# Kernel tuning notes

Hardware: AMD Instinct MI355X
Metric: run time of the kernel (lower is better)

The kernel has to match this reference:

```python
import jax, jax.numpy as jnp
import numpy as np
import math

EMBED = 1024
HEADS = 16
HEAD_DIM = EMBED // HEADS
WINDOW = 128
B, S = 2, 2048


def setup_inputs() -> dict:
    key = jax.random.key(0)
    k1, k2, k3, k4 = jax.random.split(key, 4)
    values = jax.random.normal(k1, (B, S, EMBED), dtype=jnp.float32)
    keys = jax.random.normal(k2, (B, S, EMBED), dtype=jnp.float32)
    queries = jax.random.normal(k3, (B, S, EMBED), dtype=jnp.float32)
    # sliding-window band mask: 1 where |i-j| <= WINDOW//2, else 0
    idx = jnp.arange(S)
    band = (jnp.abs(idx[:, None] - idx[None, :]) <= WINDOW // 2).astype(jnp.int32)
    mask = band[None, None, :, :]  # [1,1,S,S], broadcasts over batch and heads
    w_out = jax.random.normal(k4, (EMBED, EMBED), dtype=jnp.float32) * (1.0 / math.sqrt(EMBED))
    b_out = jnp.zeros((EMBED,), dtype=jnp.float32)
    return {"values": values, "keys": keys, "queries": queries, "mask": mask,
            "w_out": w_out, "b_out": b_out}


def reference(values, keys, queries, mask, w_out, b_out):
    N, q_len = queries.shape[0], queries.shape[1]
    v = values.reshape(N, -1, HEADS, HEAD_DIM)
    k = keys.reshape(N, -1, HEADS, HEAD_DIM)
    q = queries.reshape(N, -1, HEADS, HEAD_DIM)
    # dense N x N energy, as in the original (no windowed blocking)
    energy = jnp.einsum('nqhd,nkhd->nhqk', q, k)
    energy = jnp.where(mask == 0, jnp.float32(-1e20), energy)
    attn = jax.nn.softmax(energy / math.sqrt(EMBED), axis=3)
    out = jnp.einsum('nhql,nlhd->nqhd', attn, v).reshape(N, q_len, HEADS * HEAD_DIM)
    return out @ w_out.T + b_out
```

## Files before the change

### kernel.cpp

```cpp
#include <hip/hip_runtime.h>

typedef __bf16 bf16x8 __attribute__((ext_vector_type(8)));
typedef float floatx4 __attribute__((ext_vector_type(4)));
typedef unsigned short ushortx8 __attribute__((ext_vector_type(8)));
typedef unsigned short ushortx4 __attribute__((ext_vector_type(4)));
typedef unsigned short ushort_t;

#define SB 2048
#define EB 1024
#define HB 16
#define DB 64
#define QT 64
#define KBAND 192
#define KROW 72
#define VROW 200

__device__ __forceinline__ ushort_t f2bf(float f) {
    union { float f; unsigned int u; } v; v.f = f;
    unsigned int r = v.u + 0x7fffu + ((v.u >> 16) & 1u);
    return (ushort_t)(r >> 16);
}

union BF8 { ushortx8 u; bf16x8 b; };

__global__ __launch_bounds__(256) void cvtw_kernel(const float* __restrict__ w,
                                                   ushort_t* __restrict__ wb) {
    int i = blockIdx.x * 256 + threadIdx.x;
    const float4 v = ((const float4*)w)[i];
    ushortx4 o;
    o.x = f2bf(v.x); o.y = f2bf(v.y); o.z = f2bf(v.z); o.w = f2bf(v.w);
    ((ushortx4*)wb)[i] = o;
}

__global__ __launch_bounds__(256) void attn_kernel(const float* __restrict__ Vg,
                                                   const float* __restrict__ Kg,
                                                   const float* __restrict__ Qg,
                                                   ushort_t* __restrict__ Xg) {
    __shared__ ushort_t Klds[KBAND * KROW];
    __shared__ ushort_t Vt[DB * VROW];

    const int tid  = threadIdx.x;
    const int wave = tid >> 6;
    const int lane = tid & 63;
    const int l15  = lane & 15;
    const int l4   = lane >> 4;

    const int qt = blockIdx.x & 31;
    const int h  = (blockIdx.x >> 5) & 15;
    const int b  = blockIdx.x >> 9;

    const int q0     = qt * QT;
    const int kstart = q0 - 64;

    const float* Kbase = Kg + ((size_t)b * SB) * EB + h * DB;
    const float* Vbase = Vg + ((size_t)b * SB) * EB + h * DB;

    #pragma unroll
    for (int it = 0; it < (KBAND * DB / 4) / 256; ++it) {
        int idx = it * 256 + tid;
        int j   = idx >> 4;
        int d4  = (idx & 15) * 4;
        int kk  = kstart + j;
        float4 kv = make_float4(0.f, 0.f, 0.f, 0.f);
        float4 vv = make_float4(0.f, 0.f, 0.f, 0.f);
        if (kk >= 0 && kk < SB) {
            kv = *(const float4*)(Kbase + (size_t)kk * EB + d4);
            vv = *(const float4*)(Vbase + (size_t)kk * EB + d4);
        }
        ushortx4 ku;
        ku.x = f2bf(kv.x); ku.y = f2bf(kv.y); ku.z = f2bf(kv.z); ku.w = f2bf(kv.w);
        *(ushortx4*)(Klds + j * KROW + d4) = ku;
        Vt[(d4 + 0) * VROW + j] = f2bf(vv.x);
        Vt[(d4 + 1) * VROW + j] = f2bf(vv.y);
        Vt[(d4 + 2) * VROW + j] = f2bf(vv.z);
        Vt[(d4 + 3) * VROW + j] = f2bf(vv.w);
    }

    const int qrow = q0 + wave * 16 + l15;
    const float* Qrow = Qg + ((size_t)b * SB + qrow) * EB + h * DB;
    bf16x8 qfrag[2];
    #pragma unroll
    for (int ks = 0; ks < 2; ++ks) {
        const float4* p = (const float4*)(Qrow + ks * 32 + l4 * 8);
        float4 a0 = p[0], a1 = p[1];
        BF8 t;
        t.u[0] = f2bf(a0.x); t.u[1] = f2bf(a0.y); t.u[2] = f2bf(a0.z); t.u[3] = f2bf(a0.w);
        t.u[4] = f2bf(a1.x); t.u[5] = f2bf(a1.y); t.u[6] = f2bf(a1.z); t.u[7] = f2bf(a1.w);
        qfrag[ks] = t.b;
    }

    __syncthreads();

    floatx4 sfrag[12];
    #pragma unroll
    for (int nt = 0; nt < 12; ++nt) {
        floatx4 acc = {0.f, 0.f, 0.f, 0.f};
        #pragma unroll
        for (int ks = 0; ks < 2; ++ks) {
            bf16x8 kf = *(const bf16x8*)(Klds + (nt * 16 + l15) * KROW + ks * 32 + l4 * 8);
            acc = __builtin_amdgcn_mfma_f32_16x16x32_bf16(qfrag[ks], kf, acc, 0, 0, 0);
        }
        sfrag[nt] = acc;
    }

    const float scale = 0.03125f;
    #pragma unroll
    for (int nt = 0; nt < 12; ++nt) {
        int j = nt * 16 + l15;
        int kk = kstart + j;
        #pragma unroll
        for (int r = 0; r < 4; ++r) {
            int m = wave * 16 + l4 * 4 + r;
            bool valid = (j >= m) && (j <= m + 128) && (kk >= 0) && (kk < SB);
            float s = sfrag[nt][r] * scale;
            sfrag[nt][r] = valid ? s : -1e30f;
        }
    }
    #pragma unroll
    for (int r = 0; r < 4; ++r) {
        float mx = -1e30f;
        #pragma unroll
        for (int nt = 0; nt < 12; ++nt) mx = fmaxf(mx, sfrag[nt][r]);
        mx = fmaxf(mx, __shfl_xor(mx, 1));
        mx = fmaxf(mx, __shfl_xor(mx, 2));
        mx = fmaxf(mx, __shfl_xor(mx, 4));
        mx = fmaxf(mx, __shfl_xor(mx, 8));
        float sum = 0.f;
        #pragma unroll
        for (int nt = 0; nt < 12; ++nt) {
            float e = __expf(sfrag[nt][r] - mx);
            sfrag[nt][r] = e;
            sum += e;
        }
        sum += __shfl_xor(sum, 1);
        sum += __shfl_xor(sum, 2);
        sum += __shfl_xor(sum, 4);
        sum += __shfl_xor(sum, 8);
        float inv = 1.f / sum;
        #pragma unroll
        for (int nt = 0; nt < 12; ++nt) sfrag[nt][r] *= inv;
    }

    __syncthreads();
    ushort_t* Pw = Klds + wave * (16 * VROW);
    #pragma unroll
    for (int nt = 0; nt < 12; ++nt)
        #pragma unroll
        for (int r = 0; r < 4; ++r)
            Pw[(l4 * 4 + r) * VROW + nt * 16 + l15] = f2bf(sfrag[nt][r]);
    __syncthreads();

    #pragma unroll
    for (int nt = 0; nt < 4; ++nt) {
        floatx4 acc = {0.f, 0.f, 0.f, 0.f};
        #pragma unroll
        for (int ks = 0; ks < 6; ++ks) {
            bf16x8 pf = *(const bf16x8*)(Pw + l15 * VROW + ks * 32 + l4 * 8);
            bf16x8 vf = *(const bf16x8*)(Vt + (nt * 16 + l15) * VROW + ks * 32 + l4 * 8);
            acc = __builtin_amdgcn_mfma_f32_16x16x32_bf16(pf, vf, acc, 0, 0, 0);
        }
        #pragma unroll
        for (int r = 0; r < 4; ++r) {
            int q  = q0 + wave * 16 + l4 * 4 + r;
            int dd = h * DB + nt * 16 + l15;
            Xg[((size_t)b * SB + q) * EB + dd] = f2bf(acc[r]);
        }
    }
}

__device__ __forceinline__ void async_load16(const void* g, void* l) {
    __builtin_amdgcn_global_load_lds((__attribute__((address_space(1))) void*)g,
                                     (__attribute__((address_space(3))) void*)l,
                                     16, 0, 0);
}

__global__ __launch_bounds__(512) void proj_kernel(const ushort_t* __restrict__ X,
                                                   const ushort_t* __restrict__ Wb,
                                                   const float* __restrict__ bias,
                                                   float* __restrict__ out) {
    __shared__ ushort_t As[128 * 32];
    __shared__ ushort_t Bs[128 * 32];

    const int tid  = threadIdx.x;
    const int wave = tid >> 6;
    const int lane = tid & 63;
    const int l15  = lane & 15;
    const int l4   = lane >> 4;

    const int m0 = blockIdx.x * 128;
    const int n0 = blockIdx.y * 128;
    const int wm = (wave >> 2) * 64;
    const int wn = (wave & 3) * 32;

    floatx4 acc[4][2];
    #pragma unroll
    for (int i = 0; i < 4; ++i)
        #pragma unroll
        for (int j = 0; j < 2; ++j)
            acc[i][j] = (floatx4){0.f, 0.f, 0.f, 0.f};

    const int crow = tid >> 2;
    const int ccol = (tid & 3) * 8;
    const ushort_t* gA = X  + (size_t)(m0 + crow) * EB + ccol;
    const ushort_t* gB = Wb + (size_t)(n0 + crow) * EB + ccol;
    ushort_t* lA = As + wave * 512;
    ushort_t* lB = Bs + wave * 512;

    for (int kt = 0; kt < EB / 32; ++kt) {
        async_load16(gA, lA);
        async_load16(gB, lB);
        gA += 32; gB += 32;
        __syncthreads();

        bf16x8 af[4], bf[2];
        #pragma unroll
        for (int i = 0; i < 4; ++i)
            af[i] = *(const bf16x8*)(As + (wm + i * 16 + l15) * 32 + l4 * 8);
        #pragma unroll
        for (int j = 0; j < 2; ++j)
            bf[j] = *(const bf16x8*)(Bs + (wn + j * 16 + l15) * 32 + l4 * 8);
        #pragma unroll
        for (int i = 0; i < 4; ++i)
            #pragma unroll
            for (int j = 0; j < 2; ++j)
                acc[i][j] = __builtin_amdgcn_mfma_f32_16x16x32_bf16(af[i], bf[j], acc[i][j], 0, 0, 0);
        __syncthreads();
    }

    #pragma unroll
    for (int i = 0; i < 4; ++i)
        #pragma unroll
        for (int j = 0; j < 2; ++j)
            #pragma unroll
            for (int r = 0; r < 4; ++r) {
                int row = m0 + wm + i * 16 + l4 * 4 + r;
                int col = n0 + wn + j * 16 + l15;
                out[(size_t)row * EB + col] = acc[i][j][r] + bias[col];
            }
}

extern "C" void kernel_launch(void* const* d_in, const int* in_sizes, int n_in,
                              void* d_out, int out_size, void* d_ws, size_t ws_size,
                              hipStream_t stream) {
    const float* values  = (const float*)d_in[0];
    const float* keys    = (const float*)d_in[1];
    const float* queries = (const float*)d_in[2];
    const float* w_out   = (const float*)d_in[4];
    const float* b_out   = (const float*)d_in[5];
    float* out = (float*)d_out;

    ushort_t* X  = (ushort_t*)d_ws;
    ushort_t* Wb = (ushort_t*)d_ws + (size_t)4096 * 1024;

    cvtw_kernel<<<(EB * EB / 4) / 256, 256, 0, stream>>>(w_out, Wb);
    attn_kernel<<<2 * HB * (SB / QT), 256, 0, stream>>>(values, keys, queries, X);
    proj_kernel<<<dim3(4096 / 128, EB / 128), 512, 0, stream>>>(X, Wb, b_out, out);
}
```

Baseline: 147.7 us.

## Use 128-query attention tiles with per-wave diagonal band and retile projection GEMM

The attention kernel now handles 128 queries per block with 8 waves. Each wave computes only the 9 key tiles (and 5 PV k-steps) on its own diagonal band instead of all 12 tiles of a shared 192-key window. This cuts masked-out MFMA and softmax work and reduces redundant K/V global loads and bf16 conversion across neighbouring query tiles. The softmax scale is folded with log2(e) so exp2f can replace __expf. The output projection is retiled to 64x128 blocks with 256 threads, which doubles the grid at the cost of lower per-block reuse. The attention kernel's larger shared-memory footprint (about 78KB) and 512-thread blocks may lower occupancy.

```diff
diff --git a/kernel.cpp b/kernel.cpp
--- a/kernel.cpp
+++ b/kernel.cpp
@@ -10,10 +10,11 @@
 #define EB 1024
 #define HB 16
 #define DB 64
-#define QT 64
-#define KBAND 192
+#define QT 128
+#define KB2 256
 #define KROW 72
-#define VROW 200
+#define VROW 272
+#define PROW 168
 
 __device__ __forceinline__ ushort_t f2bf(float f) {
     union { float f; unsigned int u; } v; v.f = f;
@@ -32,11 +33,11 @@
     ((ushortx4*)wb)[i] = o;
 }
 
-__global__ __launch_bounds__(256) void attn_kernel(const float* __restrict__ Vg,
+__global__ __launch_bounds__(512) void attn_kernel(const float* __restrict__ Vg,
                                                    const float* __restrict__ Kg,
                                                    const float* __restrict__ Qg,
                                                    ushort_t* __restrict__ Xg) {
-    __shared__ ushort_t Klds[KBAND * KROW];
+    __shared__ ushort_t KP[8 * 16 * PROW];
     __shared__ ushort_t Vt[DB * VROW];
 
     const int tid  = threadIdx.x;
@@ -45,9 +46,9 @@
     const int l15  = lane & 15;
     const int l4   = lane >> 4;
 
-    const int qt = blockIdx.x & 31;
-    const int h  = (blockIdx.x >> 5) & 15;
-    const int b  = blockIdx.x >> 9;
+    const int qt = blockIdx.x & 15;
+    const int h  = (blockIdx.x >> 4) & 15;
+    const int b  = blockIdx.x >> 8;
 
     const int q0     = qt * QT;
     const int kstart = q0 - 64;
@@ -56,8 +57,8 @@
     const float* Vbase = Vg + ((size_t)b * SB) * EB + h * DB;
 
     #pragma unroll
-    for (int it = 0; it < (KBAND * DB / 4) / 256; ++it) {
-        int idx = it * 256 + tid;
+    for (int it = 0; it < (KB2 * DB / 4) / 512; ++it) {
+        int idx = it * 512 + tid;
         int j   = idx >> 4;
         int d4  = (idx & 15) * 4;
         int kk  = kstart + j;
@@ -69,11 +70,15 @@
         }
         ushortx4 ku;
         ku.x = f2bf(kv.x); ku.y = f2bf(kv.y); ku.z = f2bf(kv.z); ku.w = f2bf(kv.w);
-        *(ushortx4*)(Klds + j * KROW + d4) = ku;
+        *(ushortx4*)(KP + j * KROW + d4) = ku;
         Vt[(d4 + 0) * VROW + j] = f2bf(vv.x);
         Vt[(d4 + 1) * VROW + j] = f2bf(vv.y);
         Vt[(d4 + 2) * VROW + j] = f2bf(vv.z);
         Vt[(d4 + 3) * VROW + j] = f2bf(vv.w);
+    }
+    {
+        int r = tid >> 3, c = 256 + ((tid & 7) * 2);
+        if (r < DB) { Vt[r * VROW + c] = 0; Vt[r * VROW + c + 1] = 0; }
     }
 
     const int qrow = q0 + wave * 16 + l15;
@@ -91,28 +96,28 @@
 
     __syncthreads();
 
-    floatx4 sfrag[12];
-    #pragma unroll
-    for (int nt = 0; nt < 12; ++nt) {
+    floatx4 sfrag[9];
+    #pragma unroll
+    for (int nt = 0; nt < 9; ++nt) {
         floatx4 acc = {0.f, 0.f, 0.f, 0.f};
         #pragma unroll
         for (int ks = 0; ks < 2; ++ks) {
-            bf16x8 kf = *(const bf16x8*)(Klds + (nt * 16 + l15) * KROW + ks * 32 + l4 * 8);
+            bf16x8 kf = *(const bf16x8*)(KP + (16 * (wave + nt) + l15) * KROW + ks * 32 + l4 * 8);
             acc = __builtin_amdgcn_mfma_f32_16x16x32_bf16(qfrag[ks], kf, acc, 0, 0, 0);
         }
         sfrag[nt] = acc;
     }
 
-    const float scale = 0.03125f;
-    #pragma unroll
-    for (int nt = 0; nt < 12; ++nt) {
-        int j = nt * 16 + l15;
-        int kk = kstart + j;
+    const float scale2 = 0.04508421903306637f;
+    #pragma unroll
+    for (int nt = 0; nt < 9; ++nt) {
+        int key = kstart + 16 * (wave + nt) + l15;
         #pragma unroll
         for (int r = 0; r < 4; ++r) {
-            int m = wave * 16 + l4 * 4 + r;
-            bool valid = (j >= m) && (j <= m + 128) && (kk >= 0) && (kk < SB);
-            float s = sfrag[nt][r] * scale;
+            int m = l4 * 4 + r;
+            int d = 16 * nt + l15 - m;
+            bool valid = (d >= 0) && (d <= 128) && (key >= 0) && (key < SB);
+            float s = sfrag[nt][r] * scale2;
             sfrag[nt][r] = valid ? s : -1e30f;
         }
     }
@@ -120,15 +125,15 @@
     for (int r = 0; r < 4; ++r) {
         float mx = -1e30f;
         #pragma unroll
-        for (int nt = 0; nt < 12; ++nt) mx = fmaxf(mx, sfrag[nt][r]);
+        for (int nt = 0; nt < 9; ++nt) mx = fmaxf(mx, sfrag[nt][r]);
         mx = fmaxf(mx, __shfl_xor(mx, 1));
         mx = fmaxf(mx, __shfl_xor(mx, 2));
         mx = fmaxf(mx, __shfl_xor(mx, 4));
         mx = fmaxf(mx, __shfl_xor(mx, 8));
         float sum = 0.f;
         #pragma unroll
-        for (int nt = 0; nt < 12; ++nt) {
-            float e = __expf(sfrag[nt][r] - mx);
+        for (int nt = 0; nt < 9; ++nt) {
+            float e = exp2f(sfrag[nt][r] - mx);
             sfrag[nt][r] = e;
             sum += e;
         }
@@ -138,25 +143,33 @@
         sum += __shfl_xor(sum, 8);
         float inv = 1.f / sum;
         #pragma unroll
-        for (int nt = 0; nt < 12; ++nt) sfrag[nt][r] *= inv;
+        for (int nt = 0; nt < 9; ++nt) sfrag[nt][r] *= inv;
     }
 
     __syncthreads();
-    ushort_t* Pw = Klds + wave * (16 * VROW);
-    #pragma unroll
-    for (int nt = 0; nt < 12; ++nt)
+    ushort_t* Pw = KP + wave * (16 * PROW);
+    #pragma unroll
+    for (int nt = 0; nt < 9; ++nt)
         #pragma unroll
         for (int r = 0; r < 4; ++r)
-            Pw[(l4 * 4 + r) * VROW + nt * 16 + l15] = f2bf(sfrag[nt][r]);
+            Pw[(l4 * 4 + r) * PROW + nt * 16 + l15] = f2bf(sfrag[nt][r]);
+    #pragma unroll
+    for (int r = 0; r < 4; ++r) {
+        int row = l4 * 4 + r;
+        if (l15 < 12) {
+            Pw[row * PROW + 144 + l15 * 2]     = 0;
+            Pw[row * PROW + 144 + l15 * 2 + 1] = 0;
+        }
+    }
     __syncthreads();
 
     #pragma unroll
     for (int nt = 0; nt < 4; ++nt) {
         floatx4 acc = {0.f, 0.f, 0.f, 0.f};
         #pragma unroll
-        for (int ks = 0; ks < 6; ++ks) {
-            bf16x8 pf = *(const bf16x8*)(Pw + l15 * VROW + ks * 32 + l4 * 8);
-            bf16x8 vf = *(const bf16x8*)(Vt + (nt * 16 + l15) * VROW + ks * 32 + l4 * 8);
+        for (int ks = 0; ks < 5; ++ks) {
+            bf16x8 pf = *(const bf16x8*)(Pw + l15 * PROW + ks * 32 + l4 * 8);
+            bf16x8 vf = *(const bf16x8*)(Vt + (nt * 16 + l15) * VROW + 16 * wave + ks * 32 + l4 * 8);
             acc = __builtin_amdgcn_mfma_f32_16x16x32_bf16(pf, vf, acc, 0, 0, 0);
         }
         #pragma unroll
@@ -174,11 +187,11 @@
                                      16, 0, 0);
 }
 
-__global__ __launch_bounds__(512) void proj_kernel(const ushort_t* __restrict__ X,
+__global__ __launch_bounds__(256) void proj_kernel(const ushort_t* __restrict__ X,
                                                    const ushort_t* __restrict__ Wb,
                                                    const float* __restrict__ bias,
                                                    float* __restrict__ out) {
-    __shared__ ushort_t As[128 * 32];
+    __shared__ ushort_t As[64 * 32];
     __shared__ ushort_t Bs[128 * 32];
 
     const int tid  = threadIdx.x;
@@ -187,50 +200,53 @@
     const int l15  = lane & 15;
     const int l4   = lane >> 4;
 
-    const int m0 = blockIdx.x * 128;
+    const int m0 = blockIdx.x * 64;
     const int n0 = blockIdx.y * 128;
-    const int wm = (wave >> 2) * 64;
-    const int wn = (wave & 3) * 32;
-
-    floatx4 acc[4][2];
-    #pragma unroll
-    for (int i = 0; i < 4; ++i)
-        #pragma unroll
-        for (int j = 0; j < 2; ++j)
+    const int wm = (wave >> 1) * 32;
+    const int wn = (wave & 1) * 64;
+
+    floatx4 acc[2][4];
+    #pragma unroll
+    for (int i = 0; i < 2; ++i)
+        #pragma unroll
+        for (int j = 0; j < 4; ++j)
             acc[i][j] = (floatx4){0.f, 0.f, 0.f, 0.f};
 
-    const int crow = tid >> 2;
-    const int ccol = (tid & 3) * 8;
-    const ushort_t* gA = X  + (size_t)(m0 + crow) * EB + ccol;
-    const ushort_t* gB = Wb + (size_t)(n0 + crow) * EB + ccol;
-    ushort_t* lA = As + wave * 512;
-    ushort_t* lB = Bs + wave * 512;
+    const int cA  = wave * 64 + lane;
+    const int cB0 = wave * 128 + lane;
+    const ushort_t* gA  = X  + (size_t)(m0 + (cA >> 2)) * EB + (cA & 3) * 8;
+    const ushort_t* gB0 = Wb + (size_t)(n0 + (cB0 >> 2)) * EB + (cB0 & 3) * 8;
+    const ushort_t* gB1 = Wb + (size_t)(n0 + ((cB0 + 64) >> 2)) * EB + ((cB0 + 64) & 3) * 8;
+    ushort_t* lA  = As + wave * 512;
+    ushort_t* lB0 = Bs + wave * 1024;
+    ushort_t* lB1 = Bs + wave * 1024 + 512;
 
     for (int kt = 0; kt < EB / 32; ++kt) {
-        async_load16(gA, lA);
-        async_load16(gB, lB);
-        gA += 32; gB += 32;
+        async_load16(gA,  lA);
+        async_load16(gB0, lB0);
+        async_load16(gB1, lB1);
+        gA += 32; gB0 += 32; gB1 += 32;
         __syncthreads();
 
-        bf16x8 af[4], bf[2];
-        #pragma unroll
-        for (int i = 0; i < 4; ++i)
+        bf16x8 af[2], bfr[4];
+        #pragma unroll
+        for (int i = 0; i < 2; ++i)
             af[i] = *(const bf16x8*)(As + (wm + i * 16 + l15) * 32 + l4 * 8);
         #pragma unroll
-        for (int j = 0; j < 2; ++j)
-            bf[j] = *(const bf16x8*)(Bs + (wn + j * 16 + l15) * 32 + l4 * 8);
-        #pragma unroll
-        for (int i = 0; i < 4; ++i)
+        for (int j = 0; j < 4; ++j)
+            bfr[j] = *(const bf16x8*)(Bs + (wn + j * 16 + l15) * 32 + l4 * 8);
+        #pragma unroll
+        for (int i = 0; i < 2; ++i)
             #pragma unroll
-            for (int j = 0; j < 2; ++j)
-                acc[i][j] = __builtin_amdgcn_mfma_f32_16x16x32_bf16(af[i], bf[j], acc[i][j], 0, 0, 0);
+            for (int j = 0; j < 4; ++j)
+                acc[i][j] = __builtin_amdgcn_mfma_f32_16x16x32_bf16(af[i], bfr[j], acc[i][j], 0, 0, 0);
         __syncthreads();
     }
 
     #pragma unroll
-    for (int i = 0; i < 4; ++i)
-        #pragma unroll
-        for (int j = 0; j < 2; ++j)
+    for (int i = 0; i < 2; ++i)
+        #pragma unroll
+        for (int j = 0; j < 4; ++j)
             #pragma unroll
             for (int r = 0; r < 4; ++r) {
                 int row = m0 + wm + i * 16 + l4 * 4 + r;
@@ -249,10 +265,10 @@
     const float* b_out   = (const float*)d_in[5];
     float* out = (float*)d_out;
 
-    ushort_t* X  = (ushort_t*)d_ws;
+    ushort_t* Xb = (ushort_t*)d_ws;
     ushort_t* Wb = (ushort_t*)d_ws + (size_t)4096 * 1024;
 
     cvtw_kernel<<<(EB * EB / 4) / 256, 256, 0, stream>>>(w_out, Wb);
-    attn_kernel<<<2 * HB * (SB / QT), 256, 0, stream>>>(values, keys, queries, X);
-    proj_kernel<<<dim3(4096 / 128, EB / 128), 512, 0, stream>>>(X, Wb, b_out, out);
-}
+    attn_kernel<<<2 * HB * (SB / QT), 512, 0, stream>>>(values, keys, queries, Xb);
+    proj_kernel<<<dim3(4096 / 64, EB / 128), 256, 0, stream>>>(Xb, Wb, b_out, out);
+}
```

Result: faster. 137.2 us (-7.1%).
